# Optimization experiments

Hardware: AMD Instinct MI355X
Metric: run time of the kernel (lower is better)

## Reference

```python
import jax, jax.numpy as jnp
import numpy as np

N = 16384
F_IN = 256
F_OUT = 256


def setup_inputs() -> dict:
    key = jax.random.key(0)
    k1, k2, k3 = jax.random.split(key, 3)
    x = jax.random.normal(k1, (N, F_IN), dtype=jnp.float32)
    # dense 0/1 adjacency (original masks with adj[j] == 1)
    adj = jax.random.randint(k2, (N, N), 0, 2, dtype=jnp.int32)
    # glorot-uniform init for weight [2F_in, F_out]
    stdv = np.sqrt(6.0 / (2 * F_IN + F_OUT)).astype(np.float32)
    weight = jax.random.uniform(k3, (2 * F_IN, F_OUT), dtype=jnp.float32,
                                minval=-stdv, maxval=stdv)
    bias = jnp.zeros((F_OUT,), dtype=jnp.float32)
    return {"x": x, "adj": adj, "weight": weight, "bias": bias}


def reference(x, adj, weight, bias):
    # Mean over neighbors (adj row == 1): segment-mean expressed as a
    # normalized dense matmul -- equivalent to the per-row boolean-mask mean.
    a = adj.astype(x.dtype)                      # [N, N]
    deg = jnp.sum(a, axis=1, keepdims=True)      # [N, 1]
    x1 = (a @ x) / deg                           # [N, F] neighbor mean
    n_x = jnp.concatenate([x1, x], axis=1)       # [N, 2F]
    return n_x @ weight + bias                   # [N, F_out]
```

## Files before the change

### kernel.cpp

```cpp
#include <hip/hip_runtime.h>
#include <hip/hip_bf16.h>
#include <stdint.h>


typedef short bf16x8 __attribute__((ext_vector_type(8)));
typedef float f32x4  __attribute__((ext_vector_type(4)));

__device__ __forceinline__ uint32_t pack_bf16_rne(float lo, float hi) {
    uint32_t ul = __float_as_uint(lo);
    uint32_t uh = __float_as_uint(hi);
    ul = (ul + 0x7fffu + ((ul >> 16) & 1u)) >> 16;
    uh = (uh + 0x7fffu + ((uh >> 16) & 1u)) >> 16;
    return ul | (uh << 16);
}

__device__ __forceinline__ void gload_lds16(const void* g, void* l) {
    __builtin_amdgcn_global_load_lds(
        (__attribute__((address_space(1))) void*)g,
        (__attribute__((address_space(3))) void*)l, 16, 0, 0);
}

__global__ __launch_bounds__(256) void k_transpose_w(const float* __restrict__ w,
                                                     uint16_t* __restrict__ wt) {
    int idx = blockIdx.x * 256 + threadIdx.x;
    int n = idx >> 8;
    int k = idx & 255;
    int row = (n < 256) ? k : (256 + k);
    int col = (n < 256) ? n : (n - 256);
    uint32_t u = __float_as_uint(w[row * 256 + col]);
    u = (u + 0x7fffu + ((u >> 16) & 1u)) >> 16;
    wt[idx] = (uint16_t)u;
}

__global__ __launch_bounds__(256) void k_small_gemm(const float* __restrict__ x,
                                                    const uint16_t* __restrict__ wt,
                                                    const float* __restrict__ bias,
                                                    uint16_t* __restrict__ yT,
                                                    float* __restrict__ z) {
    __shared__ uint16_t As[128 * 32];
    __shared__ uint16_t Bs[128 * 32];

    const int t  = threadIdx.x;
    const int ct = blockIdx.x;
    const int rt = blockIdx.y;
    const int m0 = rt * 128;
    const int n0 = ct * 128;

    const int lane = t & 63, w = t >> 6;
    const int wr = w >> 1, wc = w & 1;
    const int l15 = lane & 15, quad = lane >> 4;

    f32x4 acc[4][4] = {};

    float4 a_reg[4];
    uint4  b_reg[2];

#pragma unroll
    for (int i = 0; i < 4; ++i) {
        int f4 = t + 256 * i, row = f4 >> 3, c4 = f4 & 7;
        a_reg[i] = *(const float4*)(x + (m0 + row) * 256 + c4 * 4);
    }
#pragma unroll
    for (int i = 0; i < 2; ++i) {
        int u4 = t + 256 * i, n_l = u4 >> 2, part = u4 & 3;
        b_reg[i] = *(const uint4*)(wt + (n0 + n_l) * 256 + part * 8);
    }

    for (int kk = 0; kk < 8; ++kk) {
        __syncthreads();
#pragma unroll
        for (int i = 0; i < 4; ++i) {
            int f4 = t + 256 * i, row = f4 >> 3, c4 = f4 & 7;
            uint2 p;
            p.x = pack_bf16_rne(a_reg[i].x, a_reg[i].y);
            p.y = pack_bf16_rne(a_reg[i].z, a_reg[i].w);
            *(uint2*)(As + row * 32 + c4 * 4) = p;
        }
#pragma unroll
        for (int i = 0; i < 2; ++i) {
            int u4 = t + 256 * i, n_l = u4 >> 2, part = u4 & 3;
            *(uint4*)(Bs + n_l * 32 + part * 8) = b_reg[i];
        }
        if (kk < 7) {
            int k0 = (kk + 1) * 32;
#pragma unroll
            for (int i = 0; i < 4; ++i) {
                int f4 = t + 256 * i, row = f4 >> 3, c4 = f4 & 7;
                a_reg[i] = *(const float4*)(x + (m0 + row) * 256 + k0 + c4 * 4);
            }
#pragma unroll
            for (int i = 0; i < 2; ++i) {
                int u4 = t + 256 * i, n_l = u4 >> 2, part = u4 & 3;
                b_reg[i] = *(const uint4*)(wt + (n0 + n_l) * 256 + k0 + part * 8);
            }
        }
        __syncthreads();

        bf16x8 a_frag[4], b_frag[4];
#pragma unroll
        for (int fr = 0; fr < 4; ++fr)
            a_frag[fr] = *(const bf16x8*)(As + (wr * 64 + fr * 16 + l15) * 32 + quad * 8);
#pragma unroll
        for (int fc = 0; fc < 4; ++fc)
            b_frag[fc] = *(const bf16x8*)(Bs + (wc * 64 + fc * 16 + l15) * 32 + quad * 8);
#pragma unroll
        for (int fr = 0; fr < 4; ++fr)
#pragma unroll
            for (int fc = 0; fc < 4; ++fc)
                acc[fr][fc] = __builtin_amdgcn_mfma_f32_16x16x32_bf16(
                    a_frag[fr], b_frag[fc], acc[fr][fc], 0, 0, 0);
    }

    if (ct < 2) {
#pragma unroll
        for (int fr = 0; fr < 4; ++fr) {
            int m_base = m0 + wr * 64 + fr * 16 + quad * 4;
#pragma unroll
            for (int fc = 0; fc < 4; ++fc) {
                int n_g = n0 + wc * 64 + fc * 16 + l15;
                uint2 pp;
                pp.x = pack_bf16_rne(acc[fr][fc][0], acc[fr][fc][1]);
                pp.y = pack_bf16_rne(acc[fr][fc][2], acc[fr][fc][3]);
                *(uint2*)(yT + (size_t)n_g * 16384 + m_base) = pp;
            }
        }
    } else {
#pragma unroll
        for (int fr = 0; fr < 4; ++fr) {
            int m_base = m0 + wr * 64 + fr * 16 + quad * 4;
#pragma unroll
            for (int fc = 0; fc < 4; ++fc) {
                int n_g = (n0 - 256) + wc * 64 + fc * 16 + l15;
                float bv = bias[n_g];
#pragma unroll
                for (int r = 0; r < 4; ++r)
                    z[(size_t)(m_base + r) * 256 + n_g] = acc[fr][fc][r] + bv;
            }
        }
    }
}

#define A_STRIDE 40
#define A_SZ (64 * A_STRIDE)
#define B_SZ (256 * 32)
__global__ __launch_bounds__(512, 2) void k_big_gemm(const int* __restrict__ adj,
                                                     const uint16_t* __restrict__ yT,
                                                     const float* __restrict__ z,
                                                     float* __restrict__ out) {
    __shared__ uint16_t As_f[2 * A_SZ];
    __shared__ uint16_t Bs_f[2 * B_SZ];
    __shared__ int degs[64];

    const int t = threadIdx.x;
    const int m0 = blockIdx.x * 64;
    const int lane = t & 63, w = t >> 6;
    const int wr = w >> 2, wc = w & 3;
    const int l15 = lane & 15, quad = lane >> 4;

    f32x4 acc[2][4] = {};

    const int a_n = t >> 3, a_c4 = t & 7;
    const int4* pa4 = (const int4*)(adj + (size_t)(m0 + a_n) * 16384) + a_c4;
    const int a_lds = a_n * A_STRIDE + a_c4 * 4;

    const uint16_t* pbg[2];
    int b_ldsbase[2];
#pragma unroll
    for (int i = 0; i < 2; ++i) {
        int base = (w * 2 + i) * 64;
        int s = base + lane;
        int bn = s >> 2;
        int bc = (s & 3) ^ ((bn >> 1) & 3);
        pbg[i] = yT + (size_t)bn * 16384 + bc * 8;
        b_ldsbase[i] = base * 8;
    }

#pragma unroll
    for (int i = 0; i < 2; ++i) {
        gload_lds16(pbg[i], &Bs_f[b_ldsbase[i]]);
        pbg[i] += 32;
    }
    int4 a = pa4[0]; pa4 += 8;
    int degp = a.x + a.y + a.z + a.w;
    {
        uint2 pv;
        pv.x = (uint32_t)(a.x | (a.y << 16)) * 0x3F80u;
        pv.y = (uint32_t)(a.z | (a.w << 16)) * 0x3F80u;
        *(uint2*)&As_f[a_lds] = pv;
    }
    __syncthreads();

    for (int kk = 0; kk < 512; ++kk) {
        const int p = kk & 1;
        int4 an;
        if (kk < 511) {
            an = pa4[0]; pa4 += 8;
#pragma unroll
            for (int i = 0; i < 2; ++i) {
                gload_lds16(pbg[i], &Bs_f[(1 - p) * B_SZ + b_ldsbase[i]]);
                pbg[i] += 32;
            }
        }

        const uint16_t* Ar = As_f + p * A_SZ;
        const uint16_t* Br = Bs_f + p * B_SZ;
        bf16x8 af[2], bfr[4];
#pragma unroll
        for (int fr = 0; fr < 2; ++fr) {
            int row = wr * 32 + fr * 16 + l15;
            af[fr] = *(const bf16x8*)(Ar + row * A_STRIDE + quad * 8);
        }
#pragma unroll
        for (int fc = 0; fc < 4; ++fc) {
            int n = wc * 64 + fc * 16 + l15;
            int cs = quad ^ ((n >> 1) & 3);
            bfr[fc] = *(const bf16x8*)(Br + n * 32 + cs * 8);
        }
#pragma unroll
        for (int fr = 0; fr < 2; ++fr)
#pragma unroll
            for (int fc = 0; fc < 4; ++fc)
                acc[fr][fc] = __builtin_amdgcn_mfma_f32_16x16x32_bf16(
                    af[fr], bfr[fc], acc[fr][fc], 0, 0, 0);

        if (kk < 511) {
            degp += an.x + an.y + an.z + an.w;
            uint2 pv;
            pv.x = (uint32_t)(an.x | (an.y << 16)) * 0x3F80u;
            pv.y = (uint32_t)(an.z | (an.w << 16)) * 0x3F80u;
            *(uint2*)&As_f[(1 - p) * A_SZ + a_lds] = pv;
        }
        __syncthreads();
    }

    degp += __shfl_down(degp, 4);
    degp += __shfl_down(degp, 2);
    degp += __shfl_down(degp, 1);
    if ((t & 7) == 0) degs[a_n] = degp;
    __syncthreads();

#pragma unroll
    for (int fr = 0; fr < 2; ++fr) {
#pragma unroll
        for (int r = 0; r < 4; ++r) {
            int m_l = wr * 32 + fr * 16 + quad * 4 + r;
            float inv = 1.0f / (float)degs[m_l];
            size_t mrow = (size_t)(m0 + m_l) * 256;
#pragma unroll
            for (int fc = 0; fc < 4; ++fc) {
                int n_g = wc * 64 + fc * 16 + l15;
                out[mrow + n_g] = acc[fr][fc][r] * inv + z[mrow + n_g];
            }
        }
    }
}

extern "C" void kernel_launch(void* const* d_in, const int* in_sizes, int n_in,
                              void* d_out, int out_size, void* d_ws, size_t ws_size,
                              hipStream_t stream) {
    const float* x      = (const float*)d_in[0];
    const int*   adj    = (const int*)d_in[1];
    const float* weight = (const float*)d_in[2];
    const float* bias   = (const float*)d_in[3];
    float* out = (float*)d_out;

    uint16_t* wt = (uint16_t*)d_ws;
    uint16_t* yT = (uint16_t*)((char*)d_ws + 262144);
    float*    z  = (float*)((char*)d_ws + 262144 + 8388608);

    k_transpose_w<<<512, 256, 0, stream>>>(weight, wt);
    k_small_gemm<<<dim3(4, 128), 256, 0, stream>>>(x, wt, bias, yT, z);
    k_big_gemm<<<256, 512, 0, stream>>>(adj, yT, z, out);
}
```

Baseline: 1.719 ms.

## Split big GEMM K dimension in two with a separate reduction kernel

Splits the adjacency GEMM along K into two halves launched as a 2D grid, doubling the block count from 256 to 512 so more of the GPU's CUs are busy. Each half writes partial sums and partial degrees to workspace, and a new reduce kernel combines them, applies the degree normalization and adds z. The launch bound goes to 4 blocks per CU. In exchange it adds extra global traffic for the partial buffers (32MB written and read) plus one more kernel launch.

```diff
diff --git a/kernel.cpp b/kernel.cpp
--- a/kernel.cpp
+++ b/kernel.cpp
@@ -143,16 +143,18 @@
 #define A_STRIDE 40
 #define A_SZ (64 * A_STRIDE)
 #define B_SZ (256 * 32)
-__global__ __launch_bounds__(512, 2) void k_big_gemm(const int* __restrict__ adj,
+#define KITER 256
+__global__ __launch_bounds__(512, 4) void k_big_gemm(const int* __restrict__ adj,
                                                      const uint16_t* __restrict__ yT,
-                                                     const float* __restrict__ z,
-                                                     float* __restrict__ out) {
+                                                     float* __restrict__ part,
+                                                     int* __restrict__ degw) {
     __shared__ uint16_t As_f[2 * A_SZ];
     __shared__ uint16_t Bs_f[2 * B_SZ];
-    __shared__ int degs[64];
 
     const int t = threadIdx.x;
     const int m0 = blockIdx.x * 64;
+    const int ky = blockIdx.y;
+    const int kbase = ky * 8192;
     const int lane = t & 63, w = t >> 6;
     const int wr = w >> 2, wc = w & 3;
     const int l15 = lane & 15, quad = lane >> 4;
@@ -160,7 +162,7 @@
     f32x4 acc[2][4] = {};
 
     const int a_n = t >> 3, a_c4 = t & 7;
-    const int4* pa4 = (const int4*)(adj + (size_t)(m0 + a_n) * 16384) + a_c4;
+    const int4* pa4 = (const int4*)(adj + (size_t)(m0 + a_n) * 16384 + kbase) + a_c4;
     const int a_lds = a_n * A_STRIDE + a_c4 * 4;
 
     const uint16_t* pbg[2];
@@ -171,7 +173,7 @@
         int s = base + lane;
         int bn = s >> 2;
         int bc = (s & 3) ^ ((bn >> 1) & 3);
-        pbg[i] = yT + (size_t)bn * 16384 + bc * 8;
+        pbg[i] = yT + (size_t)bn * 16384 + kbase + bc * 8;
         b_ldsbase[i] = base * 8;
     }
 
@@ -190,10 +192,10 @@
     }
     __syncthreads();
 
-    for (int kk = 0; kk < 512; ++kk) {
+    for (int kk = 0; kk < KITER; ++kk) {
         const int p = kk & 1;
         int4 an;
-        if (kk < 511) {
+        if (kk < KITER - 1) {
             an = pa4[0]; pa4 += 8;
 #pragma unroll
             for (int i = 0; i < 2; ++i) {
@@ -223,7 +225,7 @@
                 acc[fr][fc] = __builtin_amdgcn_mfma_f32_16x16x32_bf16(
                     af[fr], bfr[fc], acc[fr][fc], 0, 0, 0);
 
-        if (kk < 511) {
+        if (kk < KITER - 1) {
             degp += an.x + an.y + an.z + an.w;
             uint2 pv;
             pv.x = (uint32_t)(an.x | (an.y << 16)) * 0x3F80u;
@@ -236,23 +238,40 @@
     degp += __shfl_down(degp, 4);
     degp += __shfl_down(degp, 2);
     degp += __shfl_down(degp, 1);
-    if ((t & 7) == 0) degs[a_n] = degp;
-    __syncthreads();
-
+    if ((t & 7) == 0) degw[ky * 16384 + m0 + a_n] = degp;
+
+    float* pc = part + (size_t)ky * 16384 * 256;
 #pragma unroll
     for (int fr = 0; fr < 2; ++fr) {
 #pragma unroll
         for (int r = 0; r < 4; ++r) {
             int m_l = wr * 32 + fr * 16 + quad * 4 + r;
-            float inv = 1.0f / (float)degs[m_l];
             size_t mrow = (size_t)(m0 + m_l) * 256;
 #pragma unroll
             for (int fc = 0; fc < 4; ++fc) {
                 int n_g = wc * 64 + fc * 16 + l15;
-                out[mrow + n_g] = acc[fr][fc][r] * inv + z[mrow + n_g];
-            }
-        }
-    }
+                pc[mrow + n_g] = acc[fr][fc][r];
+            }
+        }
+    }
+}
+
+__global__ __launch_bounds__(256) void k_reduce(const float* __restrict__ part,
+                                                const int* __restrict__ degw,
+                                                const float* __restrict__ z,
+                                                float* __restrict__ out) {
+    int i4 = blockIdx.x * 256 + threadIdx.x;
+    int m = i4 >> 6;
+    float4 p0 = ((const float4*)part)[i4];
+    float4 p1 = ((const float4*)part)[i4 + 16384 * 64];
+    float4 zz = ((const float4*)z)[i4];
+    float inv = 1.0f / (float)(degw[m] + degw[16384 + m]);
+    float4 o;
+    o.x = (p0.x + p1.x) * inv + zz.x;
+    o.y = (p0.y + p1.y) * inv + zz.y;
+    o.z = (p0.z + p1.z) * inv + zz.z;
+    o.w = (p0.w + p1.w) * inv + zz.w;
+    ((float4*)out)[i4] = o;
 }
 
 extern "C" void kernel_launch(void* const* d_in, const int* in_sizes, int n_in,
@@ -264,11 +283,14 @@
     const float* bias   = (const float*)d_in[3];
     float* out = (float*)d_out;
 
-    uint16_t* wt = (uint16_t*)d_ws;
-    uint16_t* yT = (uint16_t*)((char*)d_ws + 262144);
-    float*    z  = (float*)((char*)d_ws + 262144 + 8388608);
+    uint16_t* wt   = (uint16_t*)d_ws;
+    uint16_t* yT   = (uint16_t*)((char*)d_ws + 262144);
+    float*    z    = (float*)((char*)d_ws + 262144 + 8388608);
+    float*    partb= (float*)((char*)d_ws + 262144 + 8388608 + 16777216);
+    int*      degw = (int*)((char*)d_ws + 262144 + 8388608 + 16777216 + 33554432);
 
     k_transpose_w<<<512, 256, 0, stream>>>(weight, wt);
     k_small_gemm<<<dim3(4, 128), 256, 0, stream>>>(x, wt, bias, yT, z);
-    k_big_gemm<<<256, 512, 0, stream>>>(adj, yT, z, out);
-}
+    k_big_gemm<<<dim3(256, 2), 512, 0, stream>>>(adj, yT, partb, degw);
+    k_reduce<<<4096, 256, 0, stream>>>(partb, degw, z, out);
+}
```

Result: faster. 1.525 ms (-11.3%).
